# Kernel tuning notes

Measured on AMD Instinct MI355X. Metric: run time of the kernel, lower is better.

## Reference

```python
import jax, jax.numpy as jnp
import numpy as np

N = 100000
E = 1600000
FEAT = 128
EMB = 64
HID = 64
OUT = 16


def _glorot(key, shape):
    fan_in, fan_out = shape[1], shape[0]
    lim = (6.0 / (fan_in + fan_out)) ** 0.5
    return jax.random.uniform(key, shape, jnp.float32, -lim, lim)


def setup_inputs() -> dict:
    key = jax.random.key(0)
    ks = jax.random.split(key, 16)
    return {
        "x_feat": jax.random.normal(ks[0], (N, FEAT), jnp.float32),
        "x_emb": jax.random.normal(ks[1], (N, 2, EMB), jnp.float32),
        "edge_index": jax.random.randint(ks[2], (2, E), 0, N, jnp.int32),
        # layer 0: SAGEConv(FEAT -> HID), Linear(EMB -> HID)
        "Wl0": _glorot(ks[3], (HID, FEAT)),
        "bl0": jnp.zeros((HID,), jnp.float32),
        "Wr0": _glorot(ks[4], (HID, FEAT)),
        "We0": _glorot(ks[5], (HID, EMB)),
        "be0": jnp.zeros((HID,), jnp.float32),
        # layer 1 (last): SAGEConv(HID -> OUT), Linear(EMB==HID -> OUT)
        "Wl1": _glorot(ks[6], (OUT, HID)),
        "bl1": jnp.zeros((OUT,), jnp.float32),
        "Wr1": _glorot(ks[7], (OUT, HID)),
        "We1": _glorot(ks[8], (OUT, HID)),
        "be1": jnp.zeros((OUT,), jnp.float32),
    }


def _sage_conv(x, edge_index, Wl, bl, Wr):
    # PyG SAGEConv with mean aggregation:
    #   out = lin_l(mean_{j in N(i)} x_j) + lin_r(x_i)
    src, dst = edge_index[0], edge_index[1]
    msg = x[src]                                   # [E, C] gather
    agg = jax.ops.segment_sum(msg, dst, num_segments=N)       # [N, C]
    deg = jax.ops.segment_sum(jnp.ones((E,), x.dtype), dst, num_segments=N)
    agg = agg / jnp.maximum(deg, 1.0)[:, None]     # mean over neighbors
    return agg @ Wl.T + bl + x @ Wr.T


def reference(x_feat, x_emb, edge_index,
              Wl0, bl0, Wr0, We0, be0,
              Wl1, bl1, Wr1, We1, be1):
    # forward(x=(x_feat, x_emb), edge_index=...) path, eval mode (dropout p=0)
    e = x_emb.mean(axis=1)                         # [N, EMB]
    # layer 0 (all but last): relu(sage + linear(emb))
    h = _sage_conv(x_feat, edge_index, Wl0, bl0, Wr0)
    e = e @ We0.T + be0
    h = jax.nn.relu(h + e)
    # last layer: no relu
    h = _sage_conv(h, edge_index, Wl1, bl1, Wr1)
    e = e @ We1.T + be1
    return h + e
```

## Files before the change

### kernel.cpp

```cpp
#include <hip/hip_runtime.h>
#include <hip/hip_bf16.h>
#include <cstddef>

#define NN 100000
#define EE 1600000
#define NPB 128
#define NB  782
#define ECH 4096
#define NCH 391
#define CAP 4096

typedef __attribute__((ext_vector_type(8))) short bf16x8;
typedef __attribute__((ext_vector_type(8))) unsigned short u16x8;
typedef __attribute__((ext_vector_type(4))) float f32x4;

#define YTS 72
#define RTS 68

static inline int ceil_div(int a, int b){ return (a + b - 1) / b; }

__device__ inline unsigned short f2bf(float f){
  union { float f; unsigned u; } v; v.f = f;
  unsigned r = (v.u + 0x7fff + ((v.u >> 16) & 1)) >> 16;
  return (unsigned short)r;
}
__device__ inline float bf2f(unsigned short s){
  union { unsigned u; float f; } v; v.u = ((unsigned)s) << 16;
  return v.f;
}

#define PRE_W (128 * 192)
#define PRE_E (PRE_W + 16 * 64)
#define PRE_B (PRE_E + 16)
#define PRE_C (PRE_B + 64)
#define PRE_N (PRE_C + NB)
__global__ void prep_all_kernel(const float* __restrict__ Wl0, const float* __restrict__ Wr0,
                                const float* __restrict__ We0, const float* __restrict__ bl0,
                                const float* __restrict__ be0, const float* __restrict__ We1,
                                const float* __restrict__ be1,
                                unsigned short* __restrict__ wcat, float* __restrict__ wee,
                                float* __restrict__ b1e, float* __restrict__ bias0,
                                int* __restrict__ cur){
  int idx = blockIdx.x * blockDim.x + threadIdx.x;
  if (idx < PRE_W){
    int n = idx / 192, k = idx % 192;
    float v;
    if (n < 64) v = (k < 128) ? Wl0[n * 128 + k] : 0.f;
    else        v = (k < 128) ? Wr0[(n - 64) * 128 + k] : We0[(n - 64) * 64 + (k - 128)];
    wcat[idx] = f2bf(v);
  } else if (idx < PRE_E){
    int j = idx - PRE_W;
    int i = j >> 6, c = j & 63;
    float s = 0.f;
    for (int k = 0; k < 64; k++) s += We1[i * 64 + k] * We0[k * 64 + c];
    wee[j] = s;
  } else if (idx < PRE_B){
    int i = idx - PRE_E;
    float s = be1[i];
    for (int k = 0; k < 64; k++) s += We1[i * 64 + k] * be0[k];
    b1e[i] = s;
  } else if (idx < PRE_C){
    int i = idx - PRE_B;
    bias0[i] = bl0[i] + be0[i];
  } else if (idx < PRE_N){
    cur[idx - PRE_C] = 0;
  }
}

__global__ void xprep_kernel(const float* __restrict__ xf, const float* __restrict__ xe,
                             unsigned short* __restrict__ xb){
  int g = blockIdx.x * blockDim.x + threadIdx.x;
  if (g >= NN * 24) return;
  int node = g / 24, c8 = g % 24;
  u16x8 o;
  if (c8 < 16){
    float4 a = ((const float4*)xf)[(size_t)node * 32 + c8 * 2];
    float4 b = ((const float4*)xf)[(size_t)node * 32 + c8 * 2 + 1];
    o[0]=f2bf(a.x); o[1]=f2bf(a.y); o[2]=f2bf(a.z); o[3]=f2bf(a.w);
    o[4]=f2bf(b.x); o[5]=f2bf(b.y); o[6]=f2bf(b.z); o[7]=f2bf(b.w);
  } else {
    int q = c8 - 16;
    float4 a0 = ((const float4*)xe)[(size_t)node * 32 + q * 2];
    float4 a1 = ((const float4*)xe)[(size_t)node * 32 + q * 2 + 1];
    float4 b0 = ((const float4*)xe)[(size_t)node * 32 + 16 + q * 2];
    float4 b1 = ((const float4*)xe)[(size_t)node * 32 + 16 + q * 2 + 1];
    o[0]=f2bf(0.5f*(a0.x+b0.x)); o[1]=f2bf(0.5f*(a0.y+b0.y));
    o[2]=f2bf(0.5f*(a0.z+b0.z)); o[3]=f2bf(0.5f*(a0.w+b0.w));
    o[4]=f2bf(0.5f*(a1.x+b1.x)); o[5]=f2bf(0.5f*(a1.y+b1.y));
    o[6]=f2bf(0.5f*(a1.z+b1.z)); o[7]=f2bf(0.5f*(a1.w+b1.w));
  }
  *(u16x8*)&xb[(size_t)node * 192 + c8 * 8] = o;
}

__global__ __launch_bounds__(256) void escatter_kernel(const int* __restrict__ src,
                                                       const int* __restrict__ dst,
                                                       int* __restrict__ cur,
                                                       int* __restrict__ ebkt){
  __shared__ int lh[NB];
  __shared__ int lo[NB];
  int t = threadIdx.x;
  int e0 = blockIdx.x * ECH;
  int ne = EE - e0; if (ne > ECH) ne = ECH;
  for (int i = t; i < NB; i += 256) lh[i] = 0;
  __syncthreads();
  int dl[16];
  #pragma unroll
  for (int k = 0; k < 16; k++){
    int i = t + k * 256;
    dl[k] = (i < ne) ? dst[e0 + i] : -1;
  }
  #pragma unroll
  for (int k = 0; k < 16; k++)
    if (dl[k] >= 0) atomicAdd(&lh[dl[k] >> 7], 1);
  __syncthreads();
  for (int i = t; i < NB; i += 256){
    int c = lh[i];
    lo[i] = c ? atomicAdd(&cur[i], c) : 0;
    lh[i] = 0;
  }
  __syncthreads();
  #pragma unroll
  for (int k = 0; k < 16; k++){
    int i = t + k * 256;
    if (dl[k] >= 0){
      int d = dl[k], b = d >> 7;
      int r = atomicAdd(&lh[b], 1);
      int p = lo[b] + r;
      if (p < CAP) ebkt[b * CAP + p] = ((d & 127) << 24) | src[e0 + i];
    }
  }
}

__global__ __launch_bounds__(256) void bsort_kernel(
    const int* __restrict__ cur, int* __restrict__ ebkt,
    int* __restrict__ rs, int* __restrict__ deg){
  __shared__ int lraw[CAP];
  __shared__ int lout[CAP];
  __shared__ int lh[NPB];
  __shared__ int loff[NPB];
  __shared__ int lcur[NPB];
  const int t = threadIdx.x;
  const int b = blockIdx.x;
  const int e0 = b * CAP;
  int cnt = cur[b];
  if (cnt > CAP) cnt = CAP;
  for (int i = t; i < NPB; i += 256) lh[i] = 0;
  __syncthreads();
  for (int i = t; i < cnt; i += 256){
    int w = ebkt[e0 + i];
    lraw[i] = w;
    atomicAdd(&lh[((unsigned)w) >> 24], 1);
  }
  __syncthreads();
  {
    int v = (t < NPB) ? lh[t] : 0;
    int s = v;
    for (int off = 1; off < NPB; off <<= 1){
      int x = 0;
      if (t < NPB && t >= off) x = loff[t - off];
      __syncthreads();
      if (t < NPB) loff[t] = s;
      __syncthreads();
      if (t < NPB && t >= off) s += loff[t - off];
      __syncthreads();
    }
    if (t < NPB){ loff[t] = s - v; lcur[t] = s - v; }
  }
  __syncthreads();
  for (int i = t; i < cnt; i += 256){
    int w = lraw[i];
    int d = ((unsigned)w) >> 24;
    int pos = atomicAdd(&lcur[d], 1);
    lout[pos] = w & 0xFFFFFF;
  }
  __syncthreads();
  for (int i = t; i < cnt; i += 256) ebkt[e0 + i] = lout[i];
  if (t < NPB){
    int node = b * NPB + t;
    if (node < NN){
      rs[node]  = e0 + loff[t];
      deg[node] = lh[t];
    }
  }
}

__global__ __launch_bounds__(256, 3) void l0_gemm_kernel(
    const unsigned short* __restrict__ xb, const unsigned short* __restrict__ wcat,
    unsigned short* __restrict__ y0g, float* __restrict__ re0g, int M){
  __shared__ unsigned short As[64 * 200];
  __shared__ unsigned short Ys[64 * YTS];
  __shared__ float          Rs[64 * RTS];
  const int t = threadIdx.x;
  const int row0 = blockIdx.x * 64;
  u16x8 tmp[6];
  #pragma unroll
  for (int k = 0; k < 6; k++){
    int idx = t + k * 256;
    int r = idx / 24, q = idx % 24;
    int row = row0 + r;
    u16x8 z = {0,0,0,0,0,0,0,0};
    tmp[k] = (row < M) ? *(const u16x8*)&xb[(size_t)row * 192 + q * 8] : z;
  }
  #pragma unroll
  for (int k = 0; k < 6; k++){
    int idx = t + k * 256;
    int r = idx / 24, q = idx % 24;
    *(u16x8*)&As[r * 200 + q * 8] = tmp[k];
  }
  const int w = t >> 6, l = t & 63;
  const int lm = l & 15, quad = l >> 4;
  bf16x8 bfr0[6], bfr1[6];
  {
    int n0 = w * 16 + lm;
    int n1 = 64 + w * 16 + lm;
    #pragma unroll
    for (int ks = 0; ks < 6; ks++){
      bfr0[ks] = *(const bf16x8*)&wcat[n0 * 192 + ks * 32 + quad * 8];
      bfr1[ks] = *(const bf16x8*)&wcat[n1 * 192 + ks * 32 + quad * 8];
    }
  }
  __syncthreads();
  for (int rg = 0; rg < 4; rg++){
    bf16x8 af[6];
    #pragma unroll
    for (int ks = 0; ks < 6; ks++)
      af[ks] = *(const bf16x8*)&As[(rg * 16 + lm) * 200 + ks * 32 + quad * 8];
    f32x4 acc0 = {0.f, 0.f, 0.f, 0.f};
    f32x4 acc1 = {0.f, 0.f, 0.f, 0.f};
    #pragma unroll
    for (int ks = 0; ks < 6; ks++){
      acc0 = __builtin_amdgcn_mfma_f32_16x16x32_bf16(af[ks], bfr0[ks], acc0, 0, 0, 0);
      acc1 = __builtin_amdgcn_mfma_f32_16x16x32_bf16(af[ks], bfr1[ks], acc1, 0, 0, 0);
    }
    #pragma unroll
    for (int r = 0; r < 4; r++){
      int lrow = rg * 16 + quad * 4 + r;
      Ys[lrow * YTS + w * 16 + lm] = f2bf(acc0[r]);
      Rs[lrow * RTS + w * 16 + lm] = acc1[r];
    }
  }
  __syncthreads();
  #pragma unroll
  for (int k = 0; k < 2; k++){
    int idx = t + k * 256;
    int r = idx >> 3, c8 = idx & 7;
    int grow = row0 + r;
    if (grow < M)
      *(u16x8*)&y0g[(size_t)grow * 64 + c8 * 8] = *(const u16x8*)&Ys[r * YTS + c8 * 8];
  }
  #pragma unroll
  for (int k = 0; k < 4; k++){
    int idx = t + k * 256;
    int r = idx >> 4, c4 = idx & 15;
    int grow = row0 + r;
    if (grow < M)
      *(f32x4*)&re0g[(size_t)grow * 64 + c4 * 4] = *(const f32x4*)&Rs[r * RTS + c4 * 4];
  }
}

__global__ void agg0_kernel(const unsigned short* __restrict__ y0,
                            const float* __restrict__ re0,
                            const float* __restrict__ bias0,
                            const int* __restrict__ rs, const int* __restrict__ deg,
                            const int* __restrict__ ssrc, unsigned short* __restrict__ h){
  int g = blockIdx.x * blockDim.x + threadIdx.x;
  if (g >= NN * 8) return;
  int node = g >> 3, lane = g & 7;
  int start = rs[node], cnt = deg[node];
  float acc[4][8] = {};
  int i = 0;
  for (; i + 8 <= cnt; i += 8){
    int s[8];
    #pragma unroll
    for (int j = 0; j < 8; j++) s[j] = ssrc[start + i + j];
    u16x8 v[8];
    #pragma unroll
    for (int j = 0; j < 8; j++) v[j] = *(const u16x8*)&y0[(size_t)s[j] * 64 + lane * 8];
    #pragma unroll
    for (int j = 0; j < 8; j++)
      #pragma unroll
      for (int k = 0; k < 8; k++) acc[j & 3][k] += bf2f((unsigned short)v[j][k]);
  }
  for (; i < cnt; i++){
    int s = ssrc[start + i];
    u16x8 v = *(const u16x8*)&y0[(size_t)s * 64 + lane * 8];
    #pragma unroll
    for (int k = 0; k < 8; k++) acc[0][k] += bf2f((unsigned short)v[k]);
  }
  float inv = 1.0f / (float)(cnt > 1 ? cnt : 1);
  f32x4 rv0 = *(const f32x4*)&re0[(size_t)node * 64 + lane * 8];
  f32x4 rv1 = *(const f32x4*)&re0[(size_t)node * 64 + lane * 8 + 4];
  float rvv[8] = {rv0[0], rv0[1], rv0[2], rv0[3], rv1[0], rv1[1], rv1[2], rv1[3]};
  float4 ba = ((const float4*)bias0)[lane * 2];
  float4 bb = ((const float4*)bias0)[lane * 2 + 1];
  float bv[8] = {ba.x, ba.y, ba.z, ba.w, bb.x, bb.y, bb.z, bb.w};
  u16x8 o;
  #pragma unroll
  for (int k = 0; k < 8; k++){
    float sum = (acc[0][k] + acc[1][k]) + (acc[2][k] + acc[3][k]);
    float x = sum * inv + rvv[k] + bv[k];
    o[k] = f2bf(x > 0.f ? x : 0.f);
  }
  *(u16x8*)&h[(size_t)node * 64 + lane * 8] = o;
}

__global__ __launch_bounds__(256) void gemm16_dual_kernel(
    const unsigned short* __restrict__ H, const unsigned short* __restrict__ xb,
    const float* __restrict__ Wl1, const float* __restrict__ Wr1,
    const float* __restrict__ wee,
    const float* __restrict__ bl1, const float* __restrict__ b1e,
    unsigned short* __restrict__ Y1, float* __restrict__ Out, int M){
  __shared__ float Hs[64][65];
  __shared__ float Es[64][65];
  __shared__ float Wls[16][65];
  __shared__ float Wrs[16][65];
  __shared__ float Wes[16][65];
  __shared__ float bs[16];
  const int t = threadIdx.x;
  const int row0 = blockIdx.x * 64;
  {
    int j = t >> 4, kq = t & 15;
    float4 a = ((const float4*)Wl1)[j * 16 + kq];
    float4 b = ((const float4*)Wr1)[j * 16 + kq];
    float4 c = ((const float4*)wee)[j * 16 + kq];
    Wls[j][kq*4+0]=a.x; Wls[j][kq*4+1]=a.y; Wls[j][kq*4+2]=a.z; Wls[j][kq*4+3]=a.w;
    Wrs[j][kq*4+0]=b.x; Wrs[j][kq*4+1]=b.y; Wrs[j][kq*4+2]=b.z; Wrs[j][kq*4+3]=b.w;
    Wes[j][kq*4+0]=c.x; Wes[j][kq*4+1]=c.y; Wes[j][kq*4+2]=c.z; Wes[j][kq*4+3]=c.w;
  }
  if (t < 16) bs[t] = bl1[t] + b1e[t];
  for (int idx = t; idx < 64 * 16; idx += 256){
    int n = idx >> 4, kq = idx & 15;
    int row = row0 + n;
    ushort4 hv = make_ushort4(0,0,0,0), ev = make_ushort4(0,0,0,0);
    if (row < M){
      hv = *(const ushort4*)&H[(size_t)row * 64 + kq * 4];
      ev = *(const ushort4*)&xb[(size_t)row * 192 + 128 + kq * 4];
    }
    Hs[n][kq*4+0]=bf2f(hv.x); Hs[n][kq*4+1]=bf2f(hv.y); Hs[n][kq*4+2]=bf2f(hv.z); Hs[n][kq*4+3]=bf2f(hv.w);
    Es[n][kq*4+0]=bf2f(ev.x); Es[n][kq*4+1]=bf2f(ev.y); Es[n][kq*4+2]=bf2f(ev.z); Es[n][kq*4+3]=bf2f(ev.w);
  }
  __syncthreads();
  const int n = t >> 2, jq = t & 3;
  float y[4] = {}, o[4] = {};
  #pragma unroll 4
  for (int k = 0; k < 64; k++){
    float a = Hs[n][k];
    float e = Es[n][k];
    #pragma unroll
    for (int j = 0; j < 4; j++){
      y[j] = fmaf(a, Wls[jq*4 + j][k], y[j]);
      o[j] = fmaf(a, Wrs[jq*4 + j][k], o[j]);
      o[j] = fmaf(e, Wes[jq*4 + j][k], o[j]);
    }
  }
  int row = row0 + n;
  if (row < M){
    ushort4 yb; yb.x = f2bf(y[0]); yb.y = f2bf(y[1]); yb.z = f2bf(y[2]); yb.w = f2bf(y[3]);
    *(ushort4*)&Y1[(size_t)row * 16 + jq * 4] = yb;
    ((float4*)Out)[(size_t)row * 4 + jq] =
        make_float4(o[0] + bs[jq*4+0], o[1] + bs[jq*4+1], o[2] + bs[jq*4+2], o[3] + bs[jq*4+3]);
  }
}

__global__ void agg1_kernel(const unsigned short* __restrict__ y1,
                            const int* __restrict__ rs, const int* __restrict__ deg,
                            const int* __restrict__ ssrc, float* __restrict__ outp){
  int g = blockIdx.x * blockDim.x + threadIdx.x;
  if (g >= NN * 2) return;
  int node = g >> 1, lane = g & 1;
  int start = rs[node], cnt = deg[node];
  float acc[4][8] = {};
  int i = 0;
  for (; i + 8 <= cnt; i += 8){
    int s[8];
    #pragma unroll
    for (int j = 0; j < 8; j++) s[j] = ssrc[start + i + j];
    u16x8 v[8];
    #pragma unroll
    for (int j = 0; j < 8; j++) v[j] = *(const u16x8*)&y1[(size_t)s[j] * 16 + lane * 8];
    #pragma unroll
    for (int j = 0; j < 8; j++)
      #pragma unroll
      for (int k = 0; k < 8; k++) acc[j & 3][k] += bf2f((unsigned short)v[j][k]);
  }
  for (; i < cnt; i++){
    int s = ssrc[start + i];
    u16x8 v = *(const u16x8*)&y1[(size_t)s * 16 + lane * 8];
    #pragma unroll
    for (int k = 0; k < 8; k++) acc[0][k] += bf2f((unsigned short)v[k]);
  }
  float inv = 1.0f / (float)(cnt > 1 ? cnt : 1);
  f32x4 o0 = *(f32x4*)&outp[(size_t)node * 16 + lane * 8];
  f32x4 o1 = *(f32x4*)&outp[(size_t)node * 16 + lane * 8 + 4];
  #pragma unroll
  for (int k = 0; k < 4; k++){
    o0[k] += ((acc[0][k] + acc[1][k]) + (acc[2][k] + acc[3][k])) * inv;
    o1[k] += ((acc[0][k+4] + acc[1][k+4]) + (acc[2][k+4] + acc[3][k+4])) * inv;
  }
  *(f32x4*)&outp[(size_t)node * 16 + lane * 8]     = o0;
  *(f32x4*)&outp[(size_t)node * 16 + lane * 8 + 4] = o1;
}

extern "C" void kernel_launch(void* const* d_in, const int* in_sizes, int n_in,
                              void* d_out, int out_size, void* d_ws, size_t ws_size,
                              hipStream_t stream){
  (void)in_sizes; (void)n_in; (void)out_size; (void)ws_size;
  const float* x_feat = (const float*)d_in[0];
  const float* x_emb  = (const float*)d_in[1];
  const int*   ei     = (const int*)d_in[2];
  const float* Wl0 = (const float*)d_in[3];
  const float* bl0 = (const float*)d_in[4];
  const float* Wr0 = (const float*)d_in[5];
  const float* We0 = (const float*)d_in[6];
  const float* be0 = (const float*)d_in[7];
  const float* Wl1 = (const float*)d_in[8];
  const float* bl1 = (const float*)d_in[9];
  const float* Wr1 = (const float*)d_in[10];
  const float* We1 = (const float*)d_in[11];
  const float* be1 = (const float*)d_in[12];
  float* out = (float*)d_out;

  char* w = (char*)d_ws;
  float* re0          = (float*)w;           w += sizeof(float) * (size_t)NN * 64;
  unsigned short* xb  = (unsigned short*)w;  w += sizeof(unsigned short) * (size_t)NN * 192;
  unsigned short* h   = (unsigned short*)w;  w += sizeof(unsigned short) * (size_t)NN * 64;
  unsigned short* y0  = (unsigned short*)w;  w += sizeof(unsigned short) * (size_t)NN * 64;
  unsigned short* y1  = (unsigned short*)w;  w += sizeof(unsigned short) * (size_t)NN * 16;
  unsigned short* wcat= (unsigned short*)w;  w += sizeof(unsigned short) * 128 * 192;
  float* wee   = (float*)w;                  w += sizeof(float) * 16 * 64;
  float* b1e   = (float*)w;                  w += sizeof(float) * 16;
  float* bias0 = (float*)w;                  w += sizeof(float) * 64;
  int* ebkt    = (int*)w;                    w += sizeof(int) * (size_t)NB * CAP;
  int* cur     = (int*)w;                    w += sizeof(int) * NB;
  int* rs      = (int*)w;                    w += sizeof(int) * NN;
  int* deg     = (int*)w;                    w += sizeof(int) * NN;

  const int* srcp = ei;
  const int* dstp = ei + EE;

  prep_all_kernel<<<ceil_div(PRE_N, 256), 256, 0, stream>>>(
      Wl0, Wr0, We0, bl0, be0, We1, be1, wcat, wee, b1e, bias0, cur);

  xprep_kernel<<<ceil_div(NN * 24, 256), 256, 0, stream>>>(x_feat, x_emb, xb);

  escatter_kernel<<<NCH, 256, 0, stream>>>(srcp, dstp, cur, ebkt);
  bsort_kernel<<<NB, 256, 0, stream>>>(cur, ebkt, rs, deg);

  l0_gemm_kernel<<<ceil_div(NN, 64), 256, 0, stream>>>(xb, wcat, y0, re0, NN);

  agg0_kernel<<<ceil_div(NN * 8, 256), 256, 0, stream>>>(
      y0, re0, bias0, rs, deg, ebkt, h);

  gemm16_dual_kernel<<<ceil_div(NN, 64), 256, 0, stream>>>(h, xb, Wl1, Wr1, wee,
                                                           bl1, b1e, y1, out, NN);
  agg1_kernel<<<ceil_div(NN * 2, 256), 256, 0, stream>>>(y1, rs, deg, ebkt, out);
}
```

Measured before the change: 308.4 us.

## Fuse x_feat bf16 conversion into GEMM and use per-chunk edge buckets without atomics

Removes the xprep pass over x_feat: l0_gemm now loads fp32 features and converts them to bf16 in-kernel, and only the embedding mean is precomputed into a smaller 64-wide buffer. The edge bucketing is reorganized so each chunk writes into fixed per-(chunk,bucket) slots of capacity 26, reusing the re0 buffer as scratch. bsort then gathers those slots, which drops the global atomic counter and the cur zeroing. The goal is less global traffic and fewer serialized atomics. The risk is that any chunk-bucket pair with more than 26 edges is silently truncated, which would drop edges for skewed degree distributions.

```diff
diff --git a/kernel.cpp b/kernel.cpp
--- a/kernel.cpp
+++ b/kernel.cpp
@@ -9,6 +9,7 @@
 #define ECH 4096
 #define NCH 391
 #define CAP 4096
+#define SCAP 26
 
 typedef __attribute__((ext_vector_type(8))) short bf16x8;
 typedef __attribute__((ext_vector_type(8))) unsigned short u16x8;
@@ -33,14 +34,12 @@
 #define PRE_E (PRE_W + 16 * 64)
 #define PRE_B (PRE_E + 16)
 #define PRE_C (PRE_B + 64)
-#define PRE_N (PRE_C + NB)
 __global__ void prep_all_kernel(const float* __restrict__ Wl0, const float* __restrict__ Wr0,
                                 const float* __restrict__ We0, const float* __restrict__ bl0,
                                 const float* __restrict__ be0, const float* __restrict__ We1,
                                 const float* __restrict__ be1,
                                 unsigned short* __restrict__ wcat, float* __restrict__ wee,
-                                float* __restrict__ b1e, float* __restrict__ bias0,
-                                int* __restrict__ cur){
+                                float* __restrict__ b1e, float* __restrict__ bias0){
   int idx = blockIdx.x * blockDim.x + threadIdx.x;
   if (idx < PRE_W){
     int n = idx / 192, k = idx % 192;
@@ -62,94 +61,77 @@
   } else if (idx < PRE_C){
     int i = idx - PRE_B;
     bias0[i] = bl0[i] + be0[i];
-  } else if (idx < PRE_N){
-    cur[idx - PRE_C] = 0;
-  }
-}
-
-__global__ void xprep_kernel(const float* __restrict__ xf, const float* __restrict__ xe,
-                             unsigned short* __restrict__ xb){
+  }
+}
+
+__global__ void eprep_kernel(const float* __restrict__ xe, unsigned short* __restrict__ eb){
   int g = blockIdx.x * blockDim.x + threadIdx.x;
-  if (g >= NN * 24) return;
-  int node = g / 24, c8 = g % 24;
+  if (g >= NN * 8) return;
+  int node = g >> 3, q = g & 7;
+  float4 a0 = ((const float4*)xe)[(size_t)node * 32 + q * 2];
+  float4 a1 = ((const float4*)xe)[(size_t)node * 32 + q * 2 + 1];
+  float4 b0 = ((const float4*)xe)[(size_t)node * 32 + 16 + q * 2];
+  float4 b1 = ((const float4*)xe)[(size_t)node * 32 + 16 + q * 2 + 1];
   u16x8 o;
-  if (c8 < 16){
-    float4 a = ((const float4*)xf)[(size_t)node * 32 + c8 * 2];
-    float4 b = ((const float4*)xf)[(size_t)node * 32 + c8 * 2 + 1];
-    o[0]=f2bf(a.x); o[1]=f2bf(a.y); o[2]=f2bf(a.z); o[3]=f2bf(a.w);
-    o[4]=f2bf(b.x); o[5]=f2bf(b.y); o[6]=f2bf(b.z); o[7]=f2bf(b.w);
-  } else {
-    int q = c8 - 16;
-    float4 a0 = ((const float4*)xe)[(size_t)node * 32 + q * 2];
-    float4 a1 = ((const float4*)xe)[(size_t)node * 32 + q * 2 + 1];
-    float4 b0 = ((const float4*)xe)[(size_t)node * 32 + 16 + q * 2];
-    float4 b1 = ((const float4*)xe)[(size_t)node * 32 + 16 + q * 2 + 1];
-    o[0]=f2bf(0.5f*(a0.x+b0.x)); o[1]=f2bf(0.5f*(a0.y+b0.y));
-    o[2]=f2bf(0.5f*(a0.z+b0.z)); o[3]=f2bf(0.5f*(a0.w+b0.w));
-    o[4]=f2bf(0.5f*(a1.x+b1.x)); o[5]=f2bf(0.5f*(a1.y+b1.y));
-    o[6]=f2bf(0.5f*(a1.z+b1.z)); o[7]=f2bf(0.5f*(a1.w+b1.w));
-  }
-  *(u16x8*)&xb[(size_t)node * 192 + c8 * 8] = o;
+  o[0]=f2bf(0.5f*(a0.x+b0.x)); o[1]=f2bf(0.5f*(a0.y+b0.y));
+  o[2]=f2bf(0.5f*(a0.z+b0.z)); o[3]=f2bf(0.5f*(a0.w+b0.w));
+  o[4]=f2bf(0.5f*(a1.x+b1.x)); o[5]=f2bf(0.5f*(a1.y+b1.y));
+  o[6]=f2bf(0.5f*(a1.z+b1.z)); o[7]=f2bf(0.5f*(a1.w+b1.w));
+  *(u16x8*)&eb[(size_t)node * 64 + q * 8] = o;
 }
 
 __global__ __launch_bounds__(256) void escatter_kernel(const int* __restrict__ src,
                                                        const int* __restrict__ dst,
-                                                       int* __restrict__ cur,
-                                                       int* __restrict__ ebkt){
+                                                       int* __restrict__ tmp,
+                                                       int* __restrict__ cnt){
   __shared__ int lh[NB];
-  __shared__ int lo[NB];
-  int t = threadIdx.x;
-  int e0 = blockIdx.x * ECH;
+  const int t = threadIdx.x;
+  const int c = blockIdx.x;
+  const int e0 = c * ECH;
   int ne = EE - e0; if (ne > ECH) ne = ECH;
   for (int i = t; i < NB; i += 256) lh[i] = 0;
   __syncthreads();
-  int dl[16];
   #pragma unroll
   for (int k = 0; k < 16; k++){
     int i = t + k * 256;
-    dl[k] = (i < ne) ? dst[e0 + i] : -1;
-  }
-  #pragma unroll
-  for (int k = 0; k < 16; k++)
-    if (dl[k] >= 0) atomicAdd(&lh[dl[k] >> 7], 1);
+    if (i < ne){
+      int d = dst[e0 + i];
+      int s = src[e0 + i];
+      int b = d >> 7;
+      int r = atomicAdd(&lh[b], 1);
+      if (r < SCAP)
+        tmp[((size_t)c * NB + b) * SCAP + r] = ((d & 127) << 24) | s;
+    }
+  }
   __syncthreads();
   for (int i = t; i < NB; i += 256){
-    int c = lh[i];
-    lo[i] = c ? atomicAdd(&cur[i], c) : 0;
-    lh[i] = 0;
-  }
-  __syncthreads();
-  #pragma unroll
-  for (int k = 0; k < 16; k++){
-    int i = t + k * 256;
-    if (dl[k] >= 0){
-      int d = dl[k], b = d >> 7;
-      int r = atomicAdd(&lh[b], 1);
-      int p = lo[b] + r;
-      if (p < CAP) ebkt[b * CAP + p] = ((d & 127) << 24) | src[e0 + i];
-    }
+    int v = lh[i];
+    cnt[(size_t)c * NB + i] = (v < SCAP) ? v : SCAP;
   }
 }
 
 __global__ __launch_bounds__(256) void bsort_kernel(
-    const int* __restrict__ cur, int* __restrict__ ebkt,
-    int* __restrict__ rs, int* __restrict__ deg){
-  __shared__ int lraw[CAP];
+    const int* __restrict__ tmp, const int* __restrict__ cnt,
+    int* __restrict__ ebkt, int* __restrict__ rs, int* __restrict__ deg){
+  __shared__ int lraw[NCH * SCAP];
   __shared__ int lout[CAP];
   __shared__ int lh[NPB];
   __shared__ int loff[NPB];
   __shared__ int lcur[NPB];
+  __shared__ int lcnt[NCH];
   const int t = threadIdx.x;
   const int b = blockIdx.x;
-  const int e0 = b * CAP;
-  int cnt = cur[b];
-  if (cnt > CAP) cnt = CAP;
+  for (int i = t; i < NCH; i += 256) lcnt[i] = cnt[(size_t)i * NB + b];
   for (int i = t; i < NPB; i += 256) lh[i] = 0;
   __syncthreads();
-  for (int i = t; i < cnt; i += 256){
-    int w = ebkt[e0 + i];
-    lraw[i] = w;
-    atomicAdd(&lh[((unsigned)w) >> 24], 1);
+  for (int idx = t; idx < NCH * SCAP; idx += 256){
+    int c = idx / SCAP, r = idx - c * SCAP;
+    int w = -1;
+    if (r < lcnt[c]){
+      w = tmp[((size_t)c * NB + b) * SCAP + r];
+      atomicAdd(&lh[((unsigned)w) >> 24], 1);
+    }
+    lraw[idx] = w;
   }
   __syncthreads();
   {
@@ -167,45 +149,72 @@
     if (t < NPB){ loff[t] = s - v; lcur[t] = s - v; }
   }
   __syncthreads();
-  for (int i = t; i < cnt; i += 256){
-    int w = lraw[i];
-    int d = ((unsigned)w) >> 24;
-    int pos = atomicAdd(&lcur[d], 1);
-    lout[pos] = w & 0xFFFFFF;
-  }
-  __syncthreads();
-  for (int i = t; i < cnt; i += 256) ebkt[e0 + i] = lout[i];
+  for (int idx = t; idx < NCH * SCAP; idx += 256){
+    int w = lraw[idx];
+    if (w >= 0){
+      int d = ((unsigned)w) >> 24;
+      int pos = atomicAdd(&lcur[d], 1);
+      lout[pos] = w & 0xFFFFFF;
+    }
+  }
+  __syncthreads();
+  int total = loff[NPB - 1] + lh[NPB - 1];
+  for (int i = t; i < total; i += 256) ebkt[b * CAP + i] = lout[i];
   if (t < NPB){
     int node = b * NPB + t;
     if (node < NN){
-      rs[node]  = e0 + loff[t];
+      rs[node]  = b * CAP + loff[t];
       deg[node] = lh[t];
     }
   }
 }
 
 __global__ __launch_bounds__(256, 3) void l0_gemm_kernel(
-    const unsigned short* __restrict__ xb, const unsigned short* __restrict__ wcat,
+    const float* __restrict__ xf, const unsigned short* __restrict__ eb,
+    const unsigned short* __restrict__ wcat,
     unsigned short* __restrict__ y0g, float* __restrict__ re0g, int M){
   __shared__ unsigned short As[64 * 200];
   __shared__ unsigned short Ys[64 * YTS];
   __shared__ float          Rs[64 * RTS];
   const int t = threadIdx.x;
   const int row0 = blockIdx.x * 64;
-  u16x8 tmp[6];
-  #pragma unroll
-  for (int k = 0; k < 6; k++){
-    int idx = t + k * 256;
-    int r = idx / 24, q = idx % 24;
+  float4 fa[4], fb[4];
+  u16x8 ev[2];
+  #pragma unroll
+  for (int k = 0; k < 4; k++){
+    int idx = t + k * 256;
+    int r = idx >> 4, o = idx & 15;
+    int row = row0 + r;
+    if (row < M){
+      fa[k] = ((const float4*)xf)[(size_t)row * 32 + o * 2];
+      fb[k] = ((const float4*)xf)[(size_t)row * 32 + o * 2 + 1];
+    } else {
+      fa[k] = make_float4(0.f,0.f,0.f,0.f);
+      fb[k] = make_float4(0.f,0.f,0.f,0.f);
+    }
+  }
+  #pragma unroll
+  for (int k = 0; k < 2; k++){
+    int idx = t + k * 256;
+    int r = idx >> 3, q = idx & 7;
     int row = row0 + r;
     u16x8 z = {0,0,0,0,0,0,0,0};
-    tmp[k] = (row < M) ? *(const u16x8*)&xb[(size_t)row * 192 + q * 8] : z;
-  }
-  #pragma unroll
-  for (int k = 0; k < 6; k++){
-    int idx = t + k * 256;
-    int r = idx / 24, q = idx % 24;
-    *(u16x8*)&As[r * 200 + q * 8] = tmp[k];
+    ev[k] = (row < M) ? *(const u16x8*)&eb[(size_t)row * 64 + q * 8] : z;
+  }
+  #pragma unroll
+  for (int k = 0; k < 4; k++){
+    int idx = t + k * 256;
+    int r = idx >> 4, o = idx & 15;
+    u16x8 ov;
+    ov[0]=f2bf(fa[k].x); ov[1]=f2bf(fa[k].y); ov[2]=f2bf(fa[k].z); ov[3]=f2bf(fa[k].w);
+    ov[4]=f2bf(fb[k].x); ov[5]=f2bf(fb[k].y); ov[6]=f2bf(fb[k].z); ov[7]=f2bf(fb[k].w);
+    *(u16x8*)&As[r * 200 + o * 8] = ov;
+  }
+  #pragma unroll
+  for (int k = 0; k < 2; k++){
+    int idx = t + k * 256;
+    int r = idx >> 3, q = idx & 7;
+    *(u16x8*)&As[r * 200 + 128 + q * 8] = ev[k];
   }
   const int w = t >> 6, l = t & 63;
   const int lm = l & 15, quad = l >> 4;
@@ -305,7 +314,7 @@
 }
 
 __global__ __launch_bounds__(256) void gemm16_dual_kernel(
-    const unsigned short* __restrict__ H, const unsigned short* __restrict__ xb,
+    const unsigned short* __restrict__ H, const unsigned short* __restrict__ eb,
     const float* __restrict__ Wl1, const float* __restrict__ Wr1,
     const float* __restrict__ wee,
     const float* __restrict__ bl1, const float* __restrict__ b1e,
@@ -331,13 +340,13 @@
   for (int idx = t; idx < 64 * 16; idx += 256){
     int n = idx >> 4, kq = idx & 15;
     int row = row0 + n;
-    ushort4 hv = make_ushort4(0,0,0,0), ev = make_ushort4(0,0,0,0);
+    ushort4 hv = make_ushort4(0,0,0,0), evv = make_ushort4(0,0,0,0);
     if (row < M){
-      hv = *(const ushort4*)&H[(size_t)row * 64 + kq * 4];
-      ev = *(const ushort4*)&xb[(size_t)row * 192 + 128 + kq * 4];
+      hv  = *(const ushort4*)&H[(size_t)row * 64 + kq * 4];
+      evv = *(const ushort4*)&eb[(size_t)row * 64 + kq * 4];
     }
     Hs[n][kq*4+0]=bf2f(hv.x); Hs[n][kq*4+1]=bf2f(hv.y); Hs[n][kq*4+2]=bf2f(hv.z); Hs[n][kq*4+3]=bf2f(hv.w);
-    Es[n][kq*4+0]=bf2f(ev.x); Es[n][kq*4+1]=bf2f(ev.y); Es[n][kq*4+2]=bf2f(ev.z); Es[n][kq*4+3]=bf2f(ev.w);
+    Es[n][kq*4+0]=bf2f(evv.x); Es[n][kq*4+1]=bf2f(evv.y); Es[n][kq*4+2]=bf2f(evv.z); Es[n][kq*4+3]=bf2f(evv.w);
   }
   __syncthreads();
   const int n = t >> 2, jq = t & 3;
@@ -422,36 +431,37 @@
 
   char* w = (char*)d_ws;
   float* re0          = (float*)w;           w += sizeof(float) * (size_t)NN * 64;
-  unsigned short* xb  = (unsigned short*)w;  w += sizeof(unsigned short) * (size_t)NN * 192;
+  unsigned short* y0  = (unsigned short*)w;  w += sizeof(unsigned short) * (size_t)NN * 64;
+  unsigned short* eb  = (unsigned short*)w;  w += sizeof(unsigned short) * (size_t)NN * 64;
   unsigned short* h   = (unsigned short*)w;  w += sizeof(unsigned short) * (size_t)NN * 64;
-  unsigned short* y0  = (unsigned short*)w;  w += sizeof(unsigned short) * (size_t)NN * 64;
   unsigned short* y1  = (unsigned short*)w;  w += sizeof(unsigned short) * (size_t)NN * 16;
   unsigned short* wcat= (unsigned short*)w;  w += sizeof(unsigned short) * 128 * 192;
   float* wee   = (float*)w;                  w += sizeof(float) * 16 * 64;
   float* b1e   = (float*)w;                  w += sizeof(float) * 16;
   float* bias0 = (float*)w;                  w += sizeof(float) * 64;
   int* ebkt    = (int*)w;                    w += sizeof(int) * (size_t)NB * CAP;
-  int* cur     = (int*)w;                    w += sizeof(int) * NB;
+  int* cnt     = (int*)w;                    w += sizeof(int) * (size_t)NCH * NB;
   int* rs      = (int*)w;                    w += sizeof(int) * NN;
   int* deg     = (int*)w;                    w += sizeof(int) * NN;
+  int* tmp     = (int*)re0;
 
   const int* srcp = ei;
   const int* dstp = ei + EE;
 
-  prep_all_kernel<<<ceil_div(PRE_N, 256), 256, 0, stream>>>(
-      Wl0, Wr0, We0, bl0, be0, We1, be1, wcat, wee, b1e, bias0, cur);
-
-  xprep_kernel<<<ceil_div(NN * 24, 256), 256, 0, stream>>>(x_feat, x_emb, xb);
-
-  escatter_kernel<<<NCH, 256, 0, stream>>>(srcp, dstp, cur, ebkt);
-  bsort_kernel<<<NB, 256, 0, stream>>>(cur, ebkt, rs, deg);
-
-  l0_gemm_kernel<<<ceil_div(NN, 64), 256, 0, stream>>>(xb, wcat, y0, re0, NN);
+  prep_all_kernel<<<ceil_div(PRE_C, 256), 256, 0, stream>>>(
+      Wl0, Wr0, We0, bl0, be0, We1, be1, wcat, wee, b1e, bias0);
+
+  escatter_kernel<<<NCH, 256, 0, stream>>>(srcp, dstp, tmp, cnt);
+  bsort_kernel<<<NB, 256, 0, stream>>>(tmp, cnt, ebkt, rs, deg);
+
+  eprep_kernel<<<ceil_div(NN * 8, 256), 256, 0, stream>>>(x_emb, eb);
+
+  l0_gemm_kernel<<<ceil_div(NN, 64), 256, 0, stream>>>(x_feat, eb, wcat, y0, re0, NN);
 
   agg0_kernel<<<ceil_div(NN * 8, 256), 256, 0, stream>>>(
       y0, re0, bias0, rs, deg, ebkt, h);
 
-  gemm16_dual_kernel<<<ceil_div(NN, 64), 256, 0, stream>>>(h, xb, Wl1, Wr1, wee,
+  gemm16_dual_kernel<<<ceil_div(NN, 64), 256, 0, stream>>>(h, eb, Wl1, Wr1, wee,
                                                            bl1, b1e, y1, out, NN);
   agg1_kernel<<<ceil_div(NN * 2, 256), 256, 0, stream>>>(y1, rs, deg, ebkt, out);
 }
```

Result: slower. 341.6 us (+10.8%).
